# Kernel tuning notes

Hardware: AMD Instinct MI355X
Metric: run time of the kernel (lower is better)

## Reference

```python
import jax, jax.numpy as jnp
import numpy as np
import math

B, N, D, H, A, OBS, NB = 256, 64, 512, 8, 64, 128, 4
HD = D // H
EPS = 1e-5


def layernorm(x, g, b):
    mu = jnp.mean(x, axis=-1, keepdims=True)
    var = jnp.mean((x - mu) ** 2, axis=-1, keepdims=True)
    return (x - mu) * jax.lax.rsqrt(var + EPS) * g + b


def gelu(x):
    return jax.nn.gelu(x, approximate=False)  # torch nn.GELU default = exact erf


def mha_masked(k_in, v_in, q_in, wq, wk, wv, wp, bq, bk, bv, bp):
    # weights stored [in, out]; torch Linear computes x @ W.T, same math with random init
    b, l, d = q_in.shape
    q = (q_in @ wq + bq).reshape(b, l, H, HD).transpose(0, 2, 1, 3)  # [B,H,L,hd]
    k = (k_in @ wk + bk).reshape(b, l, H, HD).transpose(0, 2, 1, 3)
    v = (v_in @ wv + bv).reshape(b, l, H, HD).transpose(0, 2, 1, 3)
    att = jnp.einsum('bhqd,bhkd->bhqk', q, k) * (1.0 / math.sqrt(HD))
    causal = jnp.tril(jnp.ones((l, l), dtype=bool))  # registered tril buffer in original MAT code
    att = jnp.where(causal[None, None], att, -jnp.inf)
    att = jax.nn.softmax(att, axis=-1)
    y = jnp.einsum('bhqk,bhkd->bhqd', att, v)
    y = y.transpose(0, 2, 1, 3).reshape(b, l, d)
    return y @ wp + bp


def setup_inputs() -> dict:
    key = jax.random.key(0)
    ks = iter(jax.random.split(key, 32))
    s = 0.02
    inp = {
        'action': jax.random.normal(next(ks), (B, N, A + 1), jnp.float32),
        'obs_rep': jax.random.normal(next(ks), (B, N, D), jnp.float32),
        'obs': jax.random.normal(next(ks), (B, N, OBS), jnp.float32),
        'w_ae': jax.random.normal(next(ks), (A + 1, D), jnp.float32) * s,
        'ln0_g': jnp.ones((D,), jnp.float32),
        'ln0_b': jnp.zeros((D,), jnp.float32),
        'blk_ln_g': jnp.ones((NB, 3, D), jnp.float32),
        'blk_ln_b': jnp.zeros((NB, 3, D), jnp.float32),
        'blk_wq': jax.random.normal(next(ks), (NB, 2, D, D), jnp.float32) * s,
        'blk_wk': jax.random.normal(next(ks), (NB, 2, D, D), jnp.float32) * s,
        'blk_wv': jax.random.normal(next(ks), (NB, 2, D, D), jnp.float32) * s,
        'blk_wp': jax.random.normal(next(ks), (NB, 2, D, D), jnp.float32) * s,
        'blk_bq': jnp.zeros((NB, 2, D), jnp.float32),
        'blk_bk': jnp.zeros((NB, 2, D), jnp.float32),
        'blk_bv': jnp.zeros((NB, 2, D), jnp.float32),
        'blk_bp': jnp.zeros((NB, 2, D), jnp.float32),
        'blk_w1': jax.random.normal(next(ks), (NB, D, D), jnp.float32) * s,
        'blk_b1': jnp.zeros((NB, D), jnp.float32),
        'blk_w2': jax.random.normal(next(ks), (NB, D, D), jnp.float32) * s,
        'blk_b2': jnp.zeros((NB, D), jnp.float32),
        'wh1': jax.random.normal(next(ks), (D, D), jnp.float32) * s,
        'bh1': jnp.zeros((D,), jnp.float32),
        'lnh_g': jnp.ones((D,), jnp.float32),
        'lnh_b': jnp.zeros((D,), jnp.float32),
        'wh2': jax.random.normal(next(ks), (D, A), jnp.float32) * s,
        'bh2': jnp.zeros((A,), jnp.float32),
    }
    return inp


def reference(action, obs_rep, obs, w_ae, ln0_g, ln0_b, blk_ln_g, blk_ln_b,
              blk_wq, blk_wk, blk_wv, blk_wp, blk_bq, blk_bk, blk_bv, blk_bp,
              blk_w1, blk_b1, blk_w2, blk_b2, wh1, bh1, lnh_g, lnh_b, wh2, bh2):
    # action encoder: Linear(no bias) + GELU, then LayerNorm
    x = layernorm(gelu(action @ w_ae), ln0_g, ln0_b)
    for i in range(NB):
        # sublayer 1: masked self-attn + residual + LN
        a1 = mha_masked(x, x, x, blk_wq[i, 0], blk_wk[i, 0], blk_wv[i, 0], blk_wp[i, 0],
                        blk_bq[i, 0], blk_bk[i, 0], blk_bv[i, 0], blk_bp[i, 0])
        x = layernorm(x + a1, blk_ln_g[i, 0], blk_ln_b[i, 0])
        # sublayer 2: masked cross-attn (key=x, value=x, query=obs_rep) + residual with obs_rep + LN
        a2 = mha_masked(x, x, obs_rep, blk_wq[i, 1], blk_wk[i, 1], blk_wv[i, 1], blk_wp[i, 1],
                        blk_bq[i, 1], blk_bk[i, 1], blk_bv[i, 1], blk_bp[i, 1])
        x = layernorm(obs_rep + a2, blk_ln_g[i, 1], blk_ln_b[i, 1])
        # sublayer 3: GELU MLP (D -> D -> D) + residual + LN
        m = gelu(x @ blk_w1[i] + blk_b1[i]) @ blk_w2[i] + blk_b2[i]
        x = layernorm(x + m, blk_ln_g[i, 2], blk_ln_b[i, 2])
    # head: Linear + GELU + LN + Linear
    h = layernorm(gelu(x @ wh1 + bh1), lnh_g, lnh_b)
    logit = h @ wh2 + bh2
    return logit
```

## Files before the change

### kernel.cpp

```cpp
#include <hip/hip_runtime.h>
#include <hip/hip_bf16.h>
#include <math.h>

namespace {

constexpr int B  = 256;
constexpr int N  = 64;
constexpr int D  = 512;
constexpr int H  = 8;
constexpr int NBLK = 4;
constexpr int M  = B * N;
constexpr float EPS = 1e-5f;
constexpr float SCALE = 0.125f;
constexpr int NEVER = 1 << 20;

typedef __attribute__((ext_vector_type(8))) short short8b;
typedef __attribute__((ext_vector_type(4))) float f32x4;

__device__ __forceinline__ float gelu_exact(float x) {
  return 0.5f * x * (1.0f + erff(x * 0.70710678118654752440f));
}

__device__ __forceinline__ unsigned short f2b_bits(float f) {
  __hip_bfloat16 h = __float2bfloat16(f);
  return *reinterpret_cast<unsigned short*>(&h);
}

#define GLOBAL_AS __attribute__((address_space(1)))
#define LDS_AS    __attribute__((address_space(3)))

__device__ __forceinline__ void gload_lds16(const void* g, void* l) {
  __builtin_amdgcn_global_load_lds((const GLOBAL_AS void*)g, (LDS_AS void*)l, 16, 0, 0);
}

template<bool GELU, int SPLIT>
__global__ __launch_bounds__(512, 2) void gemm_dp_kernel(
    const __hip_bfloat16* __restrict__ A,
    const __hip_bfloat16* __restrict__ Wt,
    const float* __restrict__ bias,
    __hip_bfloat16* __restrict__ out1, int ostr1,
    __hip_bfloat16* __restrict__ vt, int gy) {
  constexpr int K = 512;
  constexpr int NT = 8;
  __shared__ __hip_bfloat16 Als[3][128][64];
  __shared__ __hip_bfloat16 Bls[3][256][64];

  const int nwg = gridDim.x;
  const int hw  = blockIdx.x;
  const int cpx = nwg >> 3;
  const int lg  = (hw & 7) * cpx + (hw >> 3);
  const int bm  = (lg / gy) * 128;
  const int bn  = (lg % gy) * 256;

  const int tid  = threadIdx.x;
  const int wave = tid >> 6;
  const int lane = tid & 63;
  const int wm   = (wave >> 2) * 64;
  const int wn   = (wave & 3) * 64;
  const int fr   = lane & 15;
  const int fg   = lane >> 4;

  const int srow  = tid >> 3;
  const int sslot = (tid & 7) ^ (srow & 7);
  const __hip_bfloat16* gA = A  + (size_t)(bm + srow) * K + sslot * 8;
  const __hip_bfloat16* gB = Wt + (size_t)(bn + srow) * K + sslot * 8;

  auto STAGE = [&](int buf, int kt) {
    const int ko = kt * 64;
    char* la = (char*)&Als[buf][0][0] + wave * 1024;
    char* lb = (char*)&Bls[buf][0][0] + wave * 1024;
    gload_lds16(gA + ko,           la);
    gload_lds16(gA + 64 * K + ko,  la + 8192);
    gload_lds16(gB + ko,           lb);
    gload_lds16(gB + 64 * K + ko,  lb + 8192);
    gload_lds16(gB + 128 * K + ko, lb + 16384);
    gload_lds16(gB + 192 * K + ko, lb + 24576);
  };

  auto lda = [&](int buf, int mi, int ks) -> short8b {
    const int row  = wm + mi * 16 + fr;
    const int byte = row * 128 + (((ks << 2) | fg) ^ (fr & 7)) * 16;
    return *reinterpret_cast<const short8b*>((const char*)&Als[buf][0][0] + byte);
  };
  auto ldb = [&](int buf, int ni, int ks) -> short8b {
    const int row  = wn + ni * 16 + fr;
    const int byte = row * 128 + (((ks << 2) | fg) ^ (fr & 7)) * 16;
    return *reinterpret_cast<const short8b*>((const char*)&Bls[buf][0][0] + byte);
  };

  STAGE(0, 0);
  STAGE(1, 1);
  asm volatile("s_waitcnt vmcnt(6)" ::: "memory");
  __builtin_amdgcn_sched_barrier(0);
  __builtin_amdgcn_s_barrier();
  __builtin_amdgcn_sched_barrier(0);

  f32x4 acc[4][4] = {};
  for (int t = 0; t < NT; ++t) {
    const int cur = t % 3;
    if (t + 2 < NT) STAGE((t + 2) % 3, t + 2);

    short8b a0[4], b0[4], a1[4], b1[4];
#pragma unroll
    for (int mi = 0; mi < 4; ++mi) a0[mi] = lda(cur, mi, 0);
#pragma unroll
    for (int ni = 0; ni < 4; ++ni) b0[ni] = ldb(cur, ni, 0);
#pragma unroll
    for (int mi = 0; mi < 4; ++mi) a1[mi] = lda(cur, mi, 1);
#pragma unroll
    for (int ni = 0; ni < 4; ++ni) b1[ni] = ldb(cur, ni, 1);

    __builtin_amdgcn_s_setprio(1);
#pragma unroll
    for (int mi = 0; mi < 4; ++mi)
#pragma unroll
      for (int ni = 0; ni < 4; ++ni)
        acc[mi][ni] = __builtin_amdgcn_mfma_f32_16x16x32_bf16(a0[mi], b0[ni], acc[mi][ni], 0, 0, 0);
#pragma unroll
    for (int mi = 0; mi < 4; ++mi)
#pragma unroll
      for (int ni = 0; ni < 4; ++ni)
        acc[mi][ni] = __builtin_amdgcn_mfma_f32_16x16x32_bf16(a1[mi], b1[ni], acc[mi][ni], 0, 0, 0);
    __builtin_amdgcn_s_setprio(0);

    if (t + 2 < NT) {
      asm volatile("s_waitcnt vmcnt(6)" ::: "memory");
    } else {
      asm volatile("s_waitcnt vmcnt(0)" ::: "memory");
    }
    __builtin_amdgcn_sched_barrier(0);
    __builtin_amdgcn_s_barrier();
    __builtin_amdgcn_sched_barrier(0);
  }

#pragma unroll
  for (int ni = 0; ni < 4; ++ni) {
    const int col = bn + wn + ni * 16 + fr;
    const float bv = bias ? bias[col] : 0.f;
#pragma unroll
    for (int mi = 0; mi < 4; ++mi) {
      const int row0 = bm + wm + mi * 16 + fg * 4;
      if (col >= SPLIT) {
        const int vcol = col - SPLIT;
        ushort4 o;
        o.x = f2b_bits(acc[mi][ni][0] + bv);
        o.y = f2b_bits(acc[mi][ni][1] + bv);
        o.z = f2b_bits(acc[mi][ni][2] + bv);
        o.w = f2b_bits(acc[mi][ni][3] + bv);
        const int b8 = row0 >> 6, nl = row0 & 63;
        const int hh = vcol >> 6, dl = vcol & 63;
        *reinterpret_cast<ushort4*>(vt +
            ((size_t)(b8 * 8 + hh) * 4096 + dl * 64 + nl)) = o;
      } else {
#pragma unroll
        for (int q = 0; q < 4; ++q) {
          float v = acc[mi][ni][q] + bv;
          if (GELU) v = gelu_exact(v);
          out1[(size_t)(row0 + q) * ostr1 + col] = __float2bfloat16(v);
        }
      }
    }
  }
}

template<int KSTEPS>
__global__ __launch_bounds__(256) void gemm_head_kernel(
    const __hip_bfloat16* __restrict__ A,
    const __hip_bfloat16* __restrict__ Wt,
    const float* __restrict__ bias,
    float* __restrict__ out1, int ostr1, int nvalid) {
  constexpr int K = KSTEPS * 32;
  __shared__ __hip_bfloat16 Als[2][128][32];
  __shared__ __hip_bfloat16 Bls[2][128][32];

  const int bm   = blockIdx.x * 128;
  const int bn   = blockIdx.y * 128;
  const int tid  = threadIdx.x;
  const int wave = tid >> 6;
  const int lane = tid & 63;
  const int wm   = (wave >> 1) * 64;
  const int wn   = (wave & 1) * 64;
  const int fr   = lane & 15;
  const int fg   = lane >> 4;

  const int srow = (lane >> 2);
  const int scol = (lane & 3) * 8;
  const __hip_bfloat16* gA0 = A  + (size_t)(bm + wave * 32 + srow) * K + scol;
  const __hip_bfloat16* gA1 = gA0 + 16 * K;
  const __hip_bfloat16* gB0 = Wt + (size_t)(bn + wave * 32 + srow) * K + scol;
  const __hip_bfloat16* gB1 = gB0 + 16 * K;

  f32x4 acc[4][4] = {};

  auto stage = [&](int buf, int ks) {
    const int ko = ks * 32;
    gload_lds16(gA0 + ko, &Als[buf][wave * 32][0]);
    gload_lds16(gA1 + ko, &Als[buf][wave * 32 + 16][0]);
    gload_lds16(gB0 + ko, &Bls[buf][wave * 32][0]);
    gload_lds16(gB1 + ko, &Bls[buf][wave * 32 + 16][0]);
  };

  stage(0, 0);
  int buf = 0;
  for (int ks = 0; ks < KSTEPS; ++ks) {
    __syncthreads();
    if (ks + 1 < KSTEPS) stage(buf ^ 1, ks + 1);
    short8b a[4], b[4];
#pragma unroll
    for (int mi = 0; mi < 4; ++mi)
      a[mi] = *reinterpret_cast<const short8b*>(&Als[buf][wm + mi * 16 + fr][fg * 8]);
#pragma unroll
    for (int ni = 0; ni < 4; ++ni)
      b[ni] = *reinterpret_cast<const short8b*>(&Bls[buf][wn + ni * 16 + fr][fg * 8]);
#pragma unroll
    for (int mi = 0; mi < 4; ++mi)
#pragma unroll
      for (int ni = 0; ni < 4; ++ni)
        acc[mi][ni] = __builtin_amdgcn_mfma_f32_16x16x32_bf16(a[mi], b[ni], acc[mi][ni], 0, 0, 0);
    buf ^= 1;
  }

#pragma unroll
  for (int ni = 0; ni < 4; ++ni) {
    const int col = bn + wn + ni * 16 + fr;
    if (col >= nvalid) continue;
    const float bv = bias ? bias[col] : 0.f;
#pragma unroll
    for (int mi = 0; mi < 4; ++mi) {
      const int row0 = bm + wm + mi * 16 + fg * 4;
#pragma unroll
      for (int q = 0; q < 4; ++q)
        out1[(size_t)(row0 + q) * ostr1 + col] = acc[mi][ni][q] + bv;
    }
  }
}

template<int KSTEPS, bool GELU_PRE, bool RES>
__global__ __launch_bounds__(512) void gemm_ln_kernel(
    const __hip_bfloat16* __restrict__ A,
    const __hip_bfloat16* __restrict__ Wt,
    const float* __restrict__ bias,
    const __hip_bfloat16* __restrict__ resb,
    const float* __restrict__ g, const float* __restrict__ bb,
    __hip_bfloat16* __restrict__ outB) {
  constexpr int K = KSTEPS * 32;
  __shared__ __hip_bfloat16 Als[2][64][32];
  __shared__ __hip_bfloat16 Bls[2][512][32];
  __shared__ float red[64][8];
  __shared__ float mrow[64];
  __shared__ float rrow[64];

  const int bm   = blockIdx.x * 64;
  const int tid  = threadIdx.x;
  const int wave = tid >> 6;
  const int lane = tid & 63;
  const int fr   = lane & 15;
  const int fg   = lane >> 4;
  const int srow = lane >> 2;
  const int scol = (lane & 3) * 8;

  auto stage = [&](int buf, int ks) {
    const int ko = ks * 32;
    if (wave < 4)
      gload_lds16(A + (size_t)(bm + wave * 16 + srow) * K + ko + scol,
                  &Als[buf][wave * 16][0]);
#pragma unroll
    for (int c = 0; c < 4; ++c)
      gload_lds16(Wt + (size_t)(wave * 64 + c * 16 + srow) * K + ko + scol,
                  &Bls[buf][wave * 64 + c * 16][0]);
  };

  f32x4 acc[4][4] = {};
  stage(0, 0);
  int buf = 0;
  for (int ks = 0; ks < KSTEPS; ++ks) {
    __syncthreads();
    if (ks + 1 < KSTEPS) stage(buf ^ 1, ks + 1);
    short8b a[4], b[4];
#pragma unroll
    for (int mi = 0; mi < 4; ++mi)
      a[mi] = *reinterpret_cast<const short8b*>(&Als[buf][mi * 16 + fr][fg * 8]);
#pragma unroll
    for (int ni = 0; ni < 4; ++ni)
      b[ni] = *reinterpret_cast<const short8b*>(&Bls[buf][wave * 64 + ni * 16 + fr][fg * 8]);
#pragma unroll
    for (int mi = 0; mi < 4; ++mi)
#pragma unroll
      for (int ni = 0; ni < 4; ++ni)
        acc[mi][ni] = __builtin_amdgcn_mfma_f32_16x16x32_bf16(a[mi], b[ni], acc[mi][ni], 0, 0, 0);
    buf ^= 1;
  }

  float v[4][4][4];
  float bvc[4];
#pragma unroll
  for (int ni = 0; ni < 4; ++ni)
    bvc[ni] = bias ? bias[wave * 64 + ni * 16 + fr] : 0.f;
#pragma unroll
  for (int mi = 0; mi < 4; ++mi)
#pragma unroll
    for (int q = 0; q < 4; ++q) {
      const int row = bm + mi * 16 + fg * 4 + q;
#pragma unroll
      for (int ni = 0; ni < 4; ++ni) {
        float t = acc[mi][ni][q] + bvc[ni];
        if (GELU_PRE) t = gelu_exact(t);
        if (RES)
          t += __bfloat162float(resb[(size_t)row * D + wave * 64 + ni * 16 + fr]);
        v[mi][ni][q] = t;
      }
    }

  float ps[16];
#pragma unroll
  for (int mi = 0; mi < 4; ++mi)
#pragma unroll
    for (int q = 0; q < 4; ++q)
      ps[mi * 4 + q] = v[mi][0][q] + v[mi][1][q] + v[mi][2][q] + v[mi][3][q];
#pragma unroll
  for (int mask = 1; mask < 16; mask <<= 1)
#pragma unroll
    for (int t = 0; t < 16; ++t) ps[t] += __shfl_xor(ps[t], mask);
  if (fr == 0) {
#pragma unroll
    for (int mi = 0; mi < 4; ++mi)
#pragma unroll
      for (int q = 0; q < 4; ++q)
        red[mi * 16 + fg * 4 + q][wave] = ps[mi * 4 + q];
  }
  __syncthreads();
  if (tid < 64) {
    float s = 0.f;
#pragma unroll
    for (int w = 0; w < 8; ++w) s += red[tid][w];
    mrow[tid] = s * (1.f / 512.f);
  }
  __syncthreads();
  float mu[16];
#pragma unroll
  for (int mi = 0; mi < 4; ++mi)
#pragma unroll
    for (int q = 0; q < 4; ++q) mu[mi * 4 + q] = mrow[mi * 16 + fg * 4 + q];

  float ps2[16];
#pragma unroll
  for (int mi = 0; mi < 4; ++mi)
#pragma unroll
    for (int q = 0; q < 4; ++q) {
      const float m = mu[mi * 4 + q];
      float s = 0.f;
#pragma unroll
      for (int ni = 0; ni < 4; ++ni) {
        const float d = v[mi][ni][q] - m;
        s += d * d;
      }
      ps2[mi * 4 + q] = s;
    }
#pragma unroll
  for (int mask = 1; mask < 16; mask <<= 1)
#pragma unroll
    for (int t = 0; t < 16; ++t) ps2[t] += __shfl_xor(ps2[t], mask);
  if (fr == 0) {
#pragma unroll
    for (int mi = 0; mi < 4; ++mi)
#pragma unroll
      for (int q = 0; q < 4; ++q)
        red[mi * 16 + fg * 4 + q][wave] = ps2[mi * 4 + q];
  }
  __syncthreads();
  if (tid < 64) {
    float s = 0.f;
#pragma unroll
    for (int w = 0; w < 8; ++w) s += red[tid][w];
    rrow[tid] = rsqrtf(s * (1.f / 512.f) + EPS);
  }
  __syncthreads();

#pragma unroll
  for (int ni = 0; ni < 4; ++ni) {
    const int col = wave * 64 + ni * 16 + fr;
    const float gc = g[col], bc = bb[col];
#pragma unroll
    for (int mi = 0; mi < 4; ++mi)
#pragma unroll
      for (int q = 0; q < 4; ++q) {
        const int lrow = mi * 16 + fg * 4 + q;
        const int row = bm + lrow;
        const float o = (v[mi][ni][q] - mu[mi * 4 + q]) * rrow[lrow] * gc + bc;
        outB[(size_t)row * D + col] = __float2bfloat16(o);
      }
  }
}

__global__ __launch_bounds__(256) void attn_mfma_kernel(
    const __hip_bfloat16* __restrict__ qg, int qstr,
    const __hip_bfloat16* __restrict__ kg, int kstr,
    const __hip_bfloat16* __restrict__ vt,
    __hip_bfloat16* __restrict__ yg) {
  __shared__ __align__(16) char smem[33280];
  unsigned short* Qs  = (unsigned short*)smem;
  unsigned short* Ks  = (unsigned short*)(smem + 8192);
  float*          Ss  = (float*)smem;
  unsigned short* Vts = (unsigned short*)(smem + 16896);
  unsigned short* Ps  = (unsigned short*)(smem + 25088);

  const int tid  = threadIdx.x;
  const int bh   = blockIdx.x;
  const int bidx = bh >> 3, h = bh & 7;
  const size_t rbase = (size_t)bidx * 64;
  const int col0 = h * 64;

  const __hip_bfloat16* vtg = vt + (size_t)bh * 4096;
#pragma unroll
  for (int p = 0; p < 2; ++p) {
    const int idx = tid + p * 256;
    const int row = idx >> 3, c8 = (idx & 7) * 8;
    const int lb  = (row * 128 + c8 * 2) ^ ((row & 7) << 4);
    const uint4 vq = *reinterpret_cast<const uint4*>(qg + (rbase + row) * qstr + col0 + c8);
    const uint4 vk = *reinterpret_cast<const uint4*>(kg + (rbase + row) * kstr + col0 + c8);
    const uint4 vv = *reinterpret_cast<const uint4*>(vtg + idx * 8);
    *reinterpret_cast<uint4*>((char*)Qs  + lb) = vq;
    *reinterpret_cast<uint4*>((char*)Ks  + lb) = vk;
    *reinterpret_cast<uint4*>((char*)Vts + lb) = vv;
  }
  __syncthreads();

  const int wave = tid >> 6, lane = tid & 63;
  const int fr = lane & 15, fg = lane >> 4;
  const int wr = (wave >> 1) * 32, wc = (wave & 1) * 32;

  auto ldfrag = [&](const unsigned short* base, int row, int ks) -> short8b {
    const int byte = (row * 128 + ks * 64 + fg * 16) ^ ((row & 7) << 4);
    return *reinterpret_cast<const short8b*>((const char*)base + byte);
  };

  f32x4 acc[2][2] = {};
#pragma unroll
  for (int ks = 0; ks < 2; ++ks) {
    short8b a[2], b[2];
    a[0] = ldfrag(Qs, wr + fr, ks);
    a[1] = ldfrag(Qs, wr + 16 + fr, ks);
    b[0] = ldfrag(Ks, wc + fr, ks);
    b[1] = ldfrag(Ks, wc + 16 + fr, ks);
#pragma unroll
    for (int mi = 0; mi < 2; ++mi)
#pragma unroll
      for (int ni = 0; ni < 2; ++ni)
        acc[mi][ni] = __builtin_amdgcn_mfma_f32_16x16x32_bf16(a[mi], b[ni], acc[mi][ni], 0, 0, 0);
  }
  __syncthreads();

#pragma unroll
  for (int mi = 0; mi < 2; ++mi)
#pragma unroll
    for (int ni = 0; ni < 2; ++ni) {
      const int m2 = wc + ni * 16 + fr;
#pragma unroll
      for (int r = 0; r < 4; ++r) {
        const int n = wr + mi * 16 + fg * 4 + r;
        Ss[n * 66 + m2] = (m2 <= n) ? acc[mi][ni][r] * SCALE : -1e30f;
      }
    }
  __syncthreads();

  for (int n = wave * 16; n < wave * 16 + 16; ++n) {
    const float vv = Ss[n * 66 + lane];
    float mx = vv;
#pragma unroll
    for (int off = 1; off < 64; off <<= 1) mx = fmaxf(mx, __shfl_xor(mx, off));
    const float p = (lane <= n) ? __expf(vv - mx) : 0.f;
    float sum = p;
#pragma unroll
    for (int off = 1; off < 64; off <<= 1) sum += __shfl_xor(sum, off);
    const int byte = (n * 128 + lane * 2) ^ ((n & 7) << 4);
    *(unsigned short*)((char*)Ps + byte) = f2b_bits(p / sum);
  }
  __syncthreads();

  f32x4 acc2[2][2] = {};
#pragma unroll
  for (int ks = 0; ks < 2; ++ks) {
    short8b a[2], b[2];
    a[0] = ldfrag(Ps, wr + fr, ks);
    a[1] = ldfrag(Ps, wr + 16 + fr, ks);
    b[0] = ldfrag(Vts, wc + fr, ks);
    b[1] = ldfrag(Vts, wc + 16 + fr, ks);
#pragma unroll
    for (int mi = 0; mi < 2; ++mi)
#pragma unroll
      for (int ni = 0; ni < 2; ++ni)
        acc2[mi][ni] = __builtin_amdgcn_mfma_f32_16x16x32_bf16(a[mi], b[ni], acc2[mi][ni], 0, 0, 0);
  }
#pragma unroll
  for (int mi = 0; mi < 2; ++mi)
#pragma unroll
    for (int r = 0; r < 4; ++r) {
      const int n = wr + mi * 16 + fg * 4 + r;
      yg[(rbase + n) * 512 + col0 + wc + fr]      = __float2bfloat16(acc2[mi][0][r]);
      yg[(rbase + n) * 512 + col0 + wc + 16 + fr] = __float2bfloat16(acc2[mi][1][r]);
    }
}

__global__ __launch_bounds__(256) void wconv_all_kernel(
    const float* __restrict__ bwq, const float* __restrict__ bwk,
    const float* __restrict__ bwv, const float* __restrict__ bwp,
    const float* __restrict__ bw1, const float* __restrict__ bw2,
    const float* __restrict__ wh1,
    __hip_bfloat16* __restrict__ wSelf, __hip_bfloat16* __restrict__ wCq,
    __hip_bfloat16* __restrict__ wCkv, __hip_bfloat16* __restrict__ wTp,
    __hip_bfloat16* __restrict__ wTw1, __hip_bfloat16* __restrict__ wTw2,
    __hip_bfloat16* __restrict__ wTh1) {
  const size_t MAT = (size_t)D * D;
  const size_t SS = (size_t)1536 * 512, KV = (size_t)1024 * 512;
  const int z = blockIdx.z;
  const float* src;
  __hip_bfloat16* dst;
  if (z < 8)       { int i = z >> 1; src = bwq + (size_t)z * MAT;
                     dst = (z & 1) ? wCq + (size_t)i * MAT : wSelf + (size_t)i * SS; }
  else if (z < 16) { int zz = z - 8, i = zz >> 1; src = bwk + (size_t)zz * MAT;
                     dst = (zz & 1) ? wCkv + (size_t)i * KV
                                    : wSelf + (size_t)i * SS + 512 * 512; }
  else if (z < 24) { int zz = z - 16, i = zz >> 1; src = bwv + (size_t)zz * MAT;
                     dst = (zz & 1) ? wCkv + (size_t)i * KV + 512 * 512
                                    : wSelf + (size_t)i * SS + 1024 * 512; }
  else if (z < 32) { int zz = z - 24; src = bwp + (size_t)zz * MAT; dst = wTp + (size_t)zz * MAT; }
  else if (z < 36) { int zz = z - 32; src = bw1 + (size_t)zz * MAT; dst = wTw1 + (size_t)zz * MAT; }
  else if (z < 40) { int zz = z - 36; src = bw2 + (size_t)zz * MAT; dst = wTw2 + (size_t)zz * MAT; }
  else             { src = wh1; dst = wTh1; }

  __shared__ float tile[32][33];
  const int r0 = blockIdx.y * 32, c0 = blockIdx.x * 32;
  const int tr = threadIdx.x >> 5;
  const int tc = threadIdx.x & 31;
#pragma unroll
  for (int i = 0; i < 4; ++i)
    tile[tr + 8 * i][tc] = src[(size_t)(r0 + tr + 8 * i) * D + c0 + tc];
  __syncthreads();
#pragma unroll
  for (int i = 0; i < 4; ++i)
    dst[(size_t)(c0 + tr + 8 * i) * D + r0 + tc] = __float2bfloat16(tile[tc][tr + 8 * i]);
}

__global__ __launch_bounds__(256) void misc_prep_kernel(
    const float* __restrict__ w_ae, const float* __restrict__ wh2,
    const float* __restrict__ bbq, const float* __restrict__ bbk,
    const float* __restrict__ bbv, const float* __restrict__ action,
    __hip_bfloat16* __restrict__ waeT, __hip_bfloat16* __restrict__ wh2p,
    float* __restrict__ selfb, float* __restrict__ ckvb,
    float* __restrict__ bqc, __hip_bfloat16* __restrict__ actb) {
  constexpr int R0 = 512 * 96, R1 = 128 * 512, R2 = NBLK * 1536,
                R3 = NBLK * 1024, R4 = NBLK * 512, R5 = M * 96;
  constexpr int total = R0 + R1 + R2 + R3 + R4 + R5;
  for (int i = blockIdx.x * 256 + threadIdx.x; i < total; i += gridDim.x * 256) {
    int j = i;
    if (j < R0) {
      const int n = j / 96, k = j - n * 96;
      waeT[j] = (k < 65) ? __float2bfloat16(w_ae[(size_t)k * 512 + n]) : __float2bfloat16(0.f);
    } else if ((j -= R0) < R1) {
      const int n = j >> 9, k = j & 511;
      wh2p[j] = (n < 64) ? __float2bfloat16(wh2[(size_t)k * 64 + n]) : __float2bfloat16(0.f);
    } else if ((j -= R1) < R2) {
      const int blk = j / 1536, c = j - blk * 1536;
      const int seg = c >> 9, cc = c & 511;
      const float* s = (seg == 0) ? bbq : (seg == 1) ? bbk : bbv;
      selfb[j] = s[(size_t)(blk * 2) * 512 + cc];
    } else if ((j -= R2) < R3) {
      const int blk = j >> 10, c = j & 1023;
      ckvb[j] = (c < 512) ? bbk[(size_t)(blk * 2 + 1) * 512 + c]
                          : bbv[(size_t)(blk * 2 + 1) * 512 + (c - 512)];
    } else if ((j -= R3) < R4) {
      const int blk = j >> 9, c = j & 511;
      bqc[j] = bbq[(size_t)(blk * 2 + 1) * 512 + c];
    } else {
      j -= R4;
      const int row = j / 96, k = j - row * 96;
      actb[j] = (k < 65) ? __float2bfloat16(action[(size_t)row * 65 + k]) : __float2bfloat16(0.f);
    }
  }
}

__global__ __launch_bounds__(256) void cvt_kernel(
    const float* __restrict__ src, __hip_bfloat16* __restrict__ dst, int n4) {
  const int i = blockIdx.x * 256 + threadIdx.x;
  if (i < n4) {
    const float4 v = reinterpret_cast<const float4*>(src)[i];
    ushort4 o;
    o.x = f2b_bits(v.x); o.y = f2b_bits(v.y);
    o.z = f2b_bits(v.z); o.w = f2b_bits(v.w);
    reinterpret_cast<ushort4*>(dst)[i] = o;
  }
}

}

extern "C" void kernel_launch(void* const* d_in, const int* in_sizes, int n_in,
                              void* d_out, int out_size, void* d_ws, size_t ws_size,
                              hipStream_t stream) {
  const float* action  = (const float*)d_in[0];
  const float* obs_rep = (const float*)d_in[1];
  const float* w_ae    = (const float*)d_in[3];
  const float* ln0_g   = (const float*)d_in[4];
  const float* ln0_b   = (const float*)d_in[5];
  const float* bln_g   = (const float*)d_in[6];
  const float* bln_b   = (const float*)d_in[7];
  const float* bwq     = (const float*)d_in[8];
  const float* bwk     = (const float*)d_in[9];
  const float* bwv     = (const float*)d_in[10];
  const float* bwp     = (const float*)d_in[11];
  const float* bbq     = (const float*)d_in[12];
  const float* bbk     = (const float*)d_in[13];
  const float* bbv     = (const float*)d_in[14];
  const float* bbp     = (const float*)d_in[15];
  const float* bw1     = (const float*)d_in[16];
  const float* bb1     = (const float*)d_in[17];
  const float* bw2     = (const float*)d_in[18];
  const float* bb2     = (const float*)d_in[19];
  const float* wh1     = (const float*)d_in[20];
  const float* bh1     = (const float*)d_in[21];
  const float* lnh_g   = (const float*)d_in[22];
  const float* lnh_b   = (const float*)d_in[23];
  const float* wh2     = (const float*)d_in[24];
  const float* bh2     = (const float*)d_in[25];

  char* ws = (char*)d_ws;
  const size_t MAT = (size_t)D * D;
  const size_t szB = (size_t)M * D * 2;

  __hip_bfloat16* xb  = (__hip_bfloat16*)ws; ws += szB;
  __hip_bfloat16* hb  = (__hip_bfloat16*)ws; ws += szB;
  __hip_bfloat16* vtb = (__hip_bfloat16*)ws; ws += szB;
  __hip_bfloat16* orb = (__hip_bfloat16*)ws; ws += szB;
  __hip_bfloat16* qkb = (__hip_bfloat16*)ws; ws += 2 * szB;
  __hip_bfloat16* qcb = (__hip_bfloat16*)ws; ws += 4 * szB;
  __hip_bfloat16* kb  = (__hip_bfloat16*)ws; ws += szB;
  __hip_bfloat16* actb = (__hip_bfloat16*)ws; ws += (size_t)M * 96 * 2;
  __hip_bfloat16* wSelf = (__hip_bfloat16*)ws; ws += (size_t)NBLK * 1536 * 512 * 2;
  __hip_bfloat16* wCq   = (__hip_bfloat16*)ws; ws += (size_t)NBLK * 512 * 512 * 2;
  __hip_bfloat16* wCkv  = (__hip_bfloat16*)ws; ws += (size_t)NBLK * 1024 * 512 * 2;
  __hip_bfloat16* wTp   = (__hip_bfloat16*)ws; ws += 8 * MAT * 2;
  __hip_bfloat16* wTw1  = (__hip_bfloat16*)ws; ws += 4 * MAT * 2;
  __hip_bfloat16* wTw2  = (__hip_bfloat16*)ws; ws += 4 * MAT * 2;
  __hip_bfloat16* wTh1  = (__hip_bfloat16*)ws; ws += MAT * 2;
  __hip_bfloat16* wh2p  = (__hip_bfloat16*)ws; ws += 128 * 512 * 2;
  __hip_bfloat16* waeT  = (__hip_bfloat16*)ws; ws += 512 * 96 * 2;
  float* selfb         = (float*)ws;         ws += (size_t)NBLK * 1536 * 4;
  float* ckvb          = (float*)ws;         ws += (size_t)NBLK * 1024 * 4;
  float* bqc           = (float*)ws;         ws += (size_t)NBLK * 512 * 4;

  wconv_all_kernel<<<dim3(16, 16, 41), 256, 0, stream>>>(
      bwq, bwk, bwv, bwp, bw1, bw2, wh1,
      wSelf, wCq, wCkv, wTp, wTw1, wTw2, wTh1);
  misc_prep_kernel<<<2048, 256, 0, stream>>>(
      w_ae, wh2, bbq, bbk, bbv, action, waeT, wh2p, selfb, ckvb, bqc, actb);
  cvt_kernel<<<(M * D / 4 + 255) / 256, 256, 0, stream>>>(obs_rep, orb, M * D / 4);

  const size_t SS = (size_t)1536 * 512;
  const size_t KV = (size_t)1024 * 512;
  const int lnGrid = M / 64;

  gemm_ln_kernel<3, true, false><<<lnGrid, 512, 0, stream>>>(
      actb, waeT, nullptr, nullptr, ln0_g, ln0_b, xb);

  gemm_dp_kernel<false, NEVER><<<M / 128 * 8, 512, 0, stream>>>(
      orb, wCq, bqc, qcb, 2048, nullptr, 8);

  for (int i = 0; i < NBLK; ++i) {
    const float* g0 = bln_g + (size_t)(i * 3 + 0) * D;
    const float* b0 = bln_b + (size_t)(i * 3 + 0) * D;
    const float* g1 = bln_g + (size_t)(i * 3 + 1) * D;
    const float* b1 = bln_b + (size_t)(i * 3 + 1) * D;
    const float* g2 = bln_g + (size_t)(i * 3 + 2) * D;
    const float* b2 = bln_b + (size_t)(i * 3 + 2) * D;

    gemm_dp_kernel<false, 1024><<<M / 128 * 6, 512, 0, stream>>>(
        xb, wSelf + (size_t)i * SS, selfb + (size_t)i * 1536, qkb, 1024, vtb, 6);
    attn_mfma_kernel<<<B * H, 256, 0, stream>>>(qkb, 1024, qkb + 512, 1024, vtb, hb);
    gemm_ln_kernel<16, false, true><<<lnGrid, 512, 0, stream>>>(
        hb, wTp + (size_t)(i * 2) * MAT, bbp + (size_t)(i * 2) * D, xb, g0, b0, xb);

    gemm_dp_kernel<false, 512><<<M / 128 * 4, 512, 0, stream>>>(
        xb, wCkv + (size_t)i * KV, ckvb + (size_t)i * 1024, kb, 512, vtb, 4);
    attn_mfma_kernel<<<B * H, 256, 0, stream>>>(
        qcb + (size_t)i * 512, 2048, kb, 512, vtb, hb);
    gemm_ln_kernel<16, false, true><<<lnGrid, 512, 0, stream>>>(
        hb, wTp + (size_t)(i * 2 + 1) * MAT, bbp + (size_t)(i * 2 + 1) * D,
        orb, g1, b1, xb);

    gemm_dp_kernel<true, NEVER><<<M / 128 * 2, 512, 0, stream>>>(
        xb, wTw1 + (size_t)i * MAT, bb1 + (size_t)i * D, hb, 512, nullptr, 2);
    gemm_ln_kernel<16, false, true><<<lnGrid, 512, 0, stream>>>(
        hb, wTw2 + (size_t)i * MAT, bb2 + (size_t)i * D, xb, g2, b2, xb);
  }

  gemm_ln_kernel<16, true, false><<<lnGrid, 512, 0, stream>>>(
      xb, wTh1, bh1, nullptr, lnh_g, lnh_b, hb);
  gemm_head_kernel<16><<<dim3(M / 128, 1), 256, 0, stream>>>(
      hb, wh2p, bh2, (float*)d_out, 64, 64);
}
```

Before: 1.039 ms.

## Fuse MLP and head GEMM pairs through LDS, add swizzled 64-wide K tile for LN GEMMs

The MLP's two GEMMs (GELU then residual+LayerNorm) are merged into one kernel that keeps the 64x512 intermediate in swizzled LDS instead of writing it to global memory. The head's Linear+GELU+LN+Linear gets the same treatment. The projection GEMM+LN kernels now use a 64-wide K tile with XOR-swizzled LDS layout and s_setprio around the MFMA block. This removes launches and intermediate HBM traffic, but the fused kernel needs a large LDS footprint (about 64KB of mid buffer plus staging), which lowers occupancy. It also serializes the second GEMM behind the first within each block.

```diff
diff --git a/kernel.cpp b/kernel.cpp
--- a/kernel.cpp
+++ b/kernel.cpp
@@ -163,87 +163,509 @@
   }
 }
 
-template<int KSTEPS>
-__global__ __launch_bounds__(256) void gemm_head_kernel(
-    const __hip_bfloat16* __restrict__ A,
-    const __hip_bfloat16* __restrict__ Wt,
-    const float* __restrict__ bias,
-    float* __restrict__ out1, int ostr1, int nvalid) {
-  constexpr int K = KSTEPS * 32;
-  __shared__ __hip_bfloat16 Als[2][128][32];
-  __shared__ __hip_bfloat16 Bls[2][128][32];
-
-  const int bm   = blockIdx.x * 128;
-  const int bn   = blockIdx.y * 128;
-  const int tid  = threadIdx.x;
-  const int wave = tid >> 6;
-  const int lane = tid & 63;
-  const int wm   = (wave >> 1) * 64;
-  const int wn   = (wave & 1) * 64;
-  const int fr   = lane & 15;
-  const int fg   = lane >> 4;
-
-  const int srow = (lane >> 2);
-  const int scol = (lane & 3) * 8;
-  const __hip_bfloat16* gA0 = A  + (size_t)(bm + wave * 32 + srow) * K + scol;
-  const __hip_bfloat16* gA1 = gA0 + 16 * K;
-  const __hip_bfloat16* gB0 = Wt + (size_t)(bn + wave * 32 + srow) * K + scol;
-  const __hip_bfloat16* gB1 = gB0 + 16 * K;
-
-  f32x4 acc[4][4] = {};
-
-  auto stage = [&](int buf, int ks) {
-    const int ko = ks * 32;
-    gload_lds16(gA0 + ko, &Als[buf][wave * 32][0]);
-    gload_lds16(gA1 + ko, &Als[buf][wave * 32 + 16][0]);
-    gload_lds16(gB0 + ko, &Bls[buf][wave * 32][0]);
-    gload_lds16(gB1 + ko, &Bls[buf][wave * 32 + 16][0]);
-  };
-
-  stage(0, 0);
-  int buf = 0;
-  for (int ks = 0; ks < KSTEPS; ++ks) {
-    __syncthreads();
-    if (ks + 1 < KSTEPS) stage(buf ^ 1, ks + 1);
-    short8b a[4], b[4];
-#pragma unroll
-    for (int mi = 0; mi < 4; ++mi)
-      a[mi] = *reinterpret_cast<const short8b*>(&Als[buf][wm + mi * 16 + fr][fg * 8]);
-#pragma unroll
-    for (int ni = 0; ni < 4; ++ni)
-      b[ni] = *reinterpret_cast<const short8b*>(&Bls[buf][wn + ni * 16 + fr][fg * 8]);
-#pragma unroll
-    for (int mi = 0; mi < 4; ++mi)
-#pragma unroll
-      for (int ni = 0; ni < 4; ++ni)
-        acc[mi][ni] = __builtin_amdgcn_mfma_f32_16x16x32_bf16(a[mi], b[ni], acc[mi][ni], 0, 0, 0);
-    buf ^= 1;
-  }
-
-#pragma unroll
-  for (int ni = 0; ni < 4; ++ni) {
-    const int col = bn + wn + ni * 16 + fr;
-    if (col >= nvalid) continue;
-    const float bv = bias ? bias[col] : 0.f;
-#pragma unroll
-    for (int mi = 0; mi < 4; ++mi) {
-      const int row0 = bm + wm + mi * 16 + fg * 4;
-#pragma unroll
-      for (int q = 0; q < 4; ++q)
-        out1[(size_t)(row0 + q) * ostr1 + col] = acc[mi][ni][q] + bv;
-    }
-  }
-}
-
-template<int KSTEPS, bool GELU_PRE, bool RES>
-__global__ __launch_bounds__(512) void gemm_ln_kernel(
+template<bool GELU_PRE, bool RES>
+__global__ __launch_bounds__(512) void gemm_ln64_kernel(
     const __hip_bfloat16* __restrict__ A,
     const __hip_bfloat16* __restrict__ Wt,
     const float* __restrict__ bias,
     const __hip_bfloat16* __restrict__ resb,
     const float* __restrict__ g, const float* __restrict__ bb,
     __hip_bfloat16* __restrict__ outB) {
-  constexpr int K = KSTEPS * 32;
+  __shared__ __hip_bfloat16 Als[2][64][64];
+  __shared__ __hip_bfloat16 Bls[2][512][64];
+  __shared__ float red[64][8];
+  __shared__ float mrow[64];
+  __shared__ float rrow[64];
+
+  const int bm   = blockIdx.x * 64;
+  const int tid  = threadIdx.x;
+  const int wave = tid >> 6;
+  const int lane = tid & 63;
+  const int fr   = lane & 15;
+  const int fg   = lane >> 4;
+
+  const int srow  = tid >> 3;
+  const int sslot = (tid & 7) ^ (srow & 7);
+
+  auto stage = [&](int buf, int kt) {
+    const int ko = kt * 64;
+    gload_lds16(A + (size_t)(bm + srow) * 512 + ko + sslot * 8,
+                (char*)&Als[buf][0][0] + wave * 1024);
+#pragma unroll
+    for (int j = 0; j < 8; ++j) {
+      const int row = j * 64 + srow;
+      const int sl  = (tid & 7) ^ (row & 7);
+      gload_lds16(Wt + (size_t)row * 512 + ko + sl * 8,
+                  (char*)&Bls[buf][0][0] + j * 8192 + wave * 1024);
+    }
+  };
+
+  auto lda = [&](int buf, int mi, int ks) -> short8b {
+    const int row  = mi * 16 + fr;
+    const int byte = row * 128 + (((ks << 2) | fg) ^ (row & 7)) * 16;
+    return *reinterpret_cast<const short8b*>((const char*)&Als[buf][0][0] + byte);
+  };
+  auto ldb = [&](int buf, int ni, int ks) -> short8b {
+    const int row  = wave * 64 + ni * 16 + fr;
+    const int byte = row * 128 + (((ks << 2) | fg) ^ (row & 7)) * 16;
+    return *reinterpret_cast<const short8b*>((const char*)&Bls[buf][0][0] + byte);
+  };
+
+  f32x4 acc[4][4] = {};
+  stage(0, 0);
+  int buf = 0;
+  for (int kt = 0; kt < 8; ++kt) {
+    __syncthreads();
+    if (kt + 1 < 8) stage(buf ^ 1, kt + 1);
+    short8b a0[4], b0[4], a1[4], b1[4];
+#pragma unroll
+    for (int mi = 0; mi < 4; ++mi) a0[mi] = lda(buf, mi, 0);
+#pragma unroll
+    for (int ni = 0; ni < 4; ++ni) b0[ni] = ldb(buf, ni, 0);
+#pragma unroll
+    for (int mi = 0; mi < 4; ++mi) a1[mi] = lda(buf, mi, 1);
+#pragma unroll
+    for (int ni = 0; ni < 4; ++ni) b1[ni] = ldb(buf, ni, 1);
+    __builtin_amdgcn_s_setprio(1);
+#pragma unroll
+    for (int mi = 0; mi < 4; ++mi)
+#pragma unroll
+      for (int ni = 0; ni < 4; ++ni)
+        acc[mi][ni] = __builtin_amdgcn_mfma_f32_16x16x32_bf16(a0[mi], b0[ni], acc[mi][ni], 0, 0, 0);
+#pragma unroll
+    for (int mi = 0; mi < 4; ++mi)
+#pragma unroll
+      for (int ni = 0; ni < 4; ++ni)
+        acc[mi][ni] = __builtin_amdgcn_mfma_f32_16x16x32_bf16(a1[mi], b1[ni], acc[mi][ni], 0, 0, 0);
+    __builtin_amdgcn_s_setprio(0);
+    buf ^= 1;
+  }
+
+  float v[4][4][4];
+  float bvc[4];
+#pragma unroll
+  for (int ni = 0; ni < 4; ++ni)
+    bvc[ni] = bias ? bias[wave * 64 + ni * 16 + fr] : 0.f;
+#pragma unroll
+  for (int mi = 0; mi < 4; ++mi)
+#pragma unroll
+    for (int q = 0; q < 4; ++q) {
+      const int row = bm + mi * 16 + fg * 4 + q;
+#pragma unroll
+      for (int ni = 0; ni < 4; ++ni) {
+        float t = acc[mi][ni][q] + bvc[ni];
+        if (GELU_PRE) t = gelu_exact(t);
+        if (RES)
+          t += __bfloat162float(resb[(size_t)row * D + wave * 64 + ni * 16 + fr]);
+        v[mi][ni][q] = t;
+      }
+    }
+
+  float ps[16];
+#pragma unroll
+  for (int mi = 0; mi < 4; ++mi)
+#pragma unroll
+    for (int q = 0; q < 4; ++q)
+      ps[mi * 4 + q] = v[mi][0][q] + v[mi][1][q] + v[mi][2][q] + v[mi][3][q];
+#pragma unroll
+  for (int mask = 1; mask < 16; mask <<= 1)
+#pragma unroll
+    for (int t = 0; t < 16; ++t) ps[t] += __shfl_xor(ps[t], mask);
+  if (fr == 0) {
+#pragma unroll
+    for (int mi = 0; mi < 4; ++mi)
+#pragma unroll
+      for (int q = 0; q < 4; ++q)
+        red[mi * 16 + fg * 4 + q][wave] = ps[mi * 4 + q];
+  }
+  __syncthreads();
+  if (tid < 64) {
+    float s = 0.f;
+#pragma unroll
+    for (int w = 0; w < 8; ++w) s += red[tid][w];
+    mrow[tid] = s * (1.f / 512.f);
+  }
+  __syncthreads();
+  float mu[16];
+#pragma unroll
+  for (int mi = 0; mi < 4; ++mi)
+#pragma unroll
+    for (int q = 0; q < 4; ++q) mu[mi * 4 + q] = mrow[mi * 16 + fg * 4 + q];
+
+  float ps2[16];
+#pragma unroll
+  for (int mi = 0; mi < 4; ++mi)
+#pragma unroll
+    for (int q = 0; q < 4; ++q) {
+      const float m = mu[mi * 4 + q];
+      float s = 0.f;
+#pragma unroll
+      for (int ni = 0; ni < 4; ++ni) {
+        const float d = v[mi][ni][q] - m;
+        s += d * d;
+      }
+      ps2[mi * 4 + q] = s;
+    }
+#pragma unroll
+  for (int mask = 1; mask < 16; mask <<= 1)
+#pragma unroll
+    for (int t = 0; t < 16; ++t) ps2[t] += __shfl_xor(ps2[t], mask);
+  if (fr == 0) {
+#pragma unroll
+    for (int mi = 0; mi < 4; ++mi)
+#pragma unroll
+      for (int q = 0; q < 4; ++q)
+        red[mi * 16 + fg * 4 + q][wave] = ps2[mi * 4 + q];
+  }
+  __syncthreads();
+  if (tid < 64) {
+    float s = 0.f;
+#pragma unroll
+    for (int w = 0; w < 8; ++w) s += red[tid][w];
+    rrow[tid] = rsqrtf(s * (1.f / 512.f) + EPS);
+  }
+  __syncthreads();
+
+#pragma unroll
+  for (int ni = 0; ni < 4; ++ni) {
+    const int col = wave * 64 + ni * 16 + fr;
+    const float gc = g[col], bc = bb[col];
+#pragma unroll
+    for (int mi = 0; mi < 4; ++mi)
+#pragma unroll
+      for (int q = 0; q < 4; ++q) {
+        const int lrow = mi * 16 + fg * 4 + q;
+        const float o = (v[mi][ni][q] - mu[mi * 4 + q]) * rrow[lrow] * gc + bc;
+        outB[(size_t)(bm + lrow) * D + col] = __float2bfloat16(o);
+      }
+  }
+}
+
+template<int MODE>
+__global__ __launch_bounds__(512) void fused2_kernel(
+    const __hip_bfloat16* __restrict__ A,
+    const __hip_bfloat16* __restrict__ W1t, const float* __restrict__ b1,
+    const __hip_bfloat16* __restrict__ W2t, const float* __restrict__ b2,
+    const __hip_bfloat16* __restrict__ resb,
+    const float* __restrict__ g, const float* __restrict__ bb,
+    __hip_bfloat16* __restrict__ outB, float* __restrict__ outF) {
+  __shared__ __hip_bfloat16 Als[2][64][32];
+  __shared__ __hip_bfloat16 Bls[2][512][32];
+  __shared__ __hip_bfloat16 mid[64 * 512];
+  __shared__ float red[64][8];
+  __shared__ float mrow[64];
+  __shared__ float rrow[64];
+
+  const int bm   = blockIdx.x * 64;
+  const int tid  = threadIdx.x;
+  const int wave = tid >> 6;
+  const int lane = tid & 63;
+  const int fr   = lane & 15;
+  const int fg   = lane >> 4;
+
+  auto stageA = [&](int buf, int ks) {
+    if (wave < 4) {
+      const int row = wave * 16 + (lane >> 2);
+      const int sl  = (lane & 3) ^ (row & 3);
+      gload_lds16(A + (size_t)(bm + row) * 512 + ks * 32 + sl * 8,
+                  (char*)&Als[buf][0][0] + wave * 1024);
+    }
+  };
+  auto stageB = [&](const __hip_bfloat16* W, int buf, int ks) {
+#pragma unroll
+    for (int c = 0; c < 4; ++c) {
+      const int row = wave * 64 + c * 16 + (lane >> 2);
+      const int sl  = (lane & 3) ^ (row & 3);
+      gload_lds16(W + (size_t)row * 512 + ks * 32 + sl * 8,
+                  (char*)&Bls[buf][0][0] + (wave * 64 + c * 16) * 64);
+    }
+  };
+  auto stageB2h = [&](const __hip_bfloat16* W, int buf, int ks) {
+    const int row = (tid >> 2) & 127;
+    const int sl  = (tid & 3) ^ (row & 3);
+    gload_lds16(W + (size_t)row * 512 + ks * 32 + sl * 8,
+                (char*)&Bls[buf][0][0] + wave * 1024);
+  };
+
+  auto ldA = [&](int buf, int mi) -> short8b {
+    const int row  = mi * 16 + fr;
+    const int byte = row * 64 + (fg ^ (row & 3)) * 16;
+    return *reinterpret_cast<const short8b*>((const char*)&Als[buf][0][0] + byte);
+  };
+  auto ldB = [&](int buf, int row) -> short8b {
+    const int byte = row * 64 + (fg ^ (row & 3)) * 16;
+    return *reinterpret_cast<const short8b*>((const char*)&Bls[buf][0][0] + byte);
+  };
+  auto ldMid = [&](int mi, int ks) -> short8b {
+    const int row  = mi * 16 + fr;
+    const int byte = (row * 1024 + ks * 64 + fg * 16) ^ ((row & 7) << 4);
+    return *reinterpret_cast<const short8b*>((const char*)mid + byte);
+  };
+
+  f32x4 acc[4][4] = {};
+  stageA(0, 0); stageB(W1t, 0, 0);
+  int buf = 0;
+  for (int ks = 0; ks < 16; ++ks) {
+    __syncthreads();
+    if (ks + 1 < 16) { stageA(buf ^ 1, ks + 1); stageB(W1t, buf ^ 1, ks + 1); }
+    short8b a[4], b[4];
+#pragma unroll
+    for (int mi = 0; mi < 4; ++mi) a[mi] = ldA(buf, mi);
+#pragma unroll
+    for (int ni = 0; ni < 4; ++ni) b[ni] = ldB(buf, wave * 64 + ni * 16 + fr);
+#pragma unroll
+    for (int mi = 0; mi < 4; ++mi)
+#pragma unroll
+      for (int ni = 0; ni < 4; ++ni)
+        acc[mi][ni] = __builtin_amdgcn_mfma_f32_16x16x32_bf16(a[mi], b[ni], acc[mi][ni], 0, 0, 0);
+    buf ^= 1;
+  }
+
+  if (MODE == 0) stageB(W2t, 0, 0); else stageB2h(W2t, 0, 0);
+
+  {
+    float v[4][4][4];
+    float bvc[4];
+#pragma unroll
+    for (int ni = 0; ni < 4; ++ni)
+      bvc[ni] = b1[wave * 64 + ni * 16 + fr];
+#pragma unroll
+    for (int mi = 0; mi < 4; ++mi)
+#pragma unroll
+      for (int q = 0; q < 4; ++q)
+#pragma unroll
+        for (int ni = 0; ni < 4; ++ni)
+          v[mi][ni][q] = gelu_exact(acc[mi][ni][q] + bvc[ni]);
+
+    if (MODE == 1) {
+      float ps[16];
+#pragma unroll
+      for (int mi = 0; mi < 4; ++mi)
+#pragma unroll
+        for (int q = 0; q < 4; ++q)
+          ps[mi * 4 + q] = v[mi][0][q] + v[mi][1][q] + v[mi][2][q] + v[mi][3][q];
+#pragma unroll
+      for (int mask = 1; mask < 16; mask <<= 1)
+#pragma unroll
+        for (int t = 0; t < 16; ++t) ps[t] += __shfl_xor(ps[t], mask);
+      if (fr == 0)
+#pragma unroll
+        for (int mi = 0; mi < 4; ++mi)
+#pragma unroll
+          for (int q = 0; q < 4; ++q)
+            red[mi * 16 + fg * 4 + q][wave] = ps[mi * 4 + q];
+      __syncthreads();
+      if (tid < 64) {
+        float s = 0.f;
+#pragma unroll
+        for (int w = 0; w < 8; ++w) s += red[tid][w];
+        mrow[tid] = s * (1.f / 512.f);
+      }
+      __syncthreads();
+      float mu[16];
+#pragma unroll
+      for (int mi = 0; mi < 4; ++mi)
+#pragma unroll
+        for (int q = 0; q < 4; ++q) mu[mi * 4 + q] = mrow[mi * 16 + fg * 4 + q];
+      float ps2[16];
+#pragma unroll
+      for (int mi = 0; mi < 4; ++mi)
+#pragma unroll
+        for (int q = 0; q < 4; ++q) {
+          const float m = mu[mi * 4 + q];
+          float s = 0.f;
+#pragma unroll
+          for (int ni = 0; ni < 4; ++ni) { const float d = v[mi][ni][q] - m; s += d * d; }
+          ps2[mi * 4 + q] = s;
+        }
+#pragma unroll
+      for (int mask = 1; mask < 16; mask <<= 1)
+#pragma unroll
+        for (int t = 0; t < 16; ++t) ps2[t] += __shfl_xor(ps2[t], mask);
+      if (fr == 0)
+#pragma unroll
+        for (int mi = 0; mi < 4; ++mi)
+#pragma unroll
+          for (int q = 0; q < 4; ++q)
+            red[mi * 16 + fg * 4 + q][wave] = ps2[mi * 4 + q];
+      __syncthreads();
+      if (tid < 64) {
+        float s = 0.f;
+#pragma unroll
+        for (int w = 0; w < 8; ++w) s += red[tid][w];
+        rrow[tid] = rsqrtf(s * (1.f / 512.f) + EPS);
+      }
+      __syncthreads();
+#pragma unroll
+      for (int mi = 0; mi < 4; ++mi)
+#pragma unroll
+        for (int q = 0; q < 4; ++q) {
+          const int lrow = mi * 16 + fg * 4 + q;
+#pragma unroll
+          for (int ni = 0; ni < 4; ++ni) {
+            const int col = wave * 64 + ni * 16 + fr;
+            v[mi][ni][q] = (v[mi][ni][q] - mu[mi * 4 + q]) * rrow[lrow] * g[col] + bb[col];
+          }
+        }
+    }
+
+#pragma unroll
+    for (int mi = 0; mi < 4; ++mi)
+#pragma unroll
+      for (int q = 0; q < 4; ++q) {
+        const int row = mi * 16 + fg * 4 + q;
+#pragma unroll
+        for (int ni = 0; ni < 4; ++ni) {
+          const int col = wave * 64 + ni * 16 + fr;
+          const int byte = (row * 1024 + col * 2) ^ ((row & 7) << 4);
+          *(unsigned short*)((char*)mid + byte) = f2b_bits(v[mi][ni][q]);
+        }
+      }
+  }
+  __syncthreads();
+
+  if (MODE == 0) {
+    f32x4 acc2[4][4] = {};
+    int buf2 = 0;
+    for (int ks = 0; ks < 16; ++ks) {
+      if (ks) __syncthreads();
+      if (ks + 1 < 16) stageB(W2t, buf2 ^ 1, ks + 1);
+      short8b a[4], b[4];
+#pragma unroll
+      for (int mi = 0; mi < 4; ++mi) a[mi] = ldMid(mi, ks);
+#pragma unroll
+      for (int ni = 0; ni < 4; ++ni) b[ni] = ldB(buf2, wave * 64 + ni * 16 + fr);
+#pragma unroll
+      for (int mi = 0; mi < 4; ++mi)
+#pragma unroll
+        for (int ni = 0; ni < 4; ++ni)
+          acc2[mi][ni] = __builtin_amdgcn_mfma_f32_16x16x32_bf16(a[mi], b[ni], acc2[mi][ni], 0, 0, 0);
+      buf2 ^= 1;
+    }
+    __syncthreads();
+
+    float v[4][4][4];
+    float bvc[4];
+#pragma unroll
+    for (int ni = 0; ni < 4; ++ni)
+      bvc[ni] = b2[wave * 64 + ni * 16 + fr];
+#pragma unroll
+    for (int mi = 0; mi < 4; ++mi)
+#pragma unroll
+      for (int q = 0; q < 4; ++q) {
+        const int row = bm + mi * 16 + fg * 4 + q;
+#pragma unroll
+        for (int ni = 0; ni < 4; ++ni)
+          v[mi][ni][q] = acc2[mi][ni][q] + bvc[ni] +
+              __bfloat162float(resb[(size_t)row * D + wave * 64 + ni * 16 + fr]);
+      }
+
+    float ps[16];
+#pragma unroll
+    for (int mi = 0; mi < 4; ++mi)
+#pragma unroll
+      for (int q = 0; q < 4; ++q)
+        ps[mi * 4 + q] = v[mi][0][q] + v[mi][1][q] + v[mi][2][q] + v[mi][3][q];
+#pragma unroll
+    for (int mask = 1; mask < 16; mask <<= 1)
+#pragma unroll
+      for (int t = 0; t < 16; ++t) ps[t] += __shfl_xor(ps[t], mask);
+    if (fr == 0)
+#pragma unroll
+      for (int mi = 0; mi < 4; ++mi)
+#pragma unroll
+        for (int q = 0; q < 4; ++q)
+          red[mi * 16 + fg * 4 + q][wave] = ps[mi * 4 + q];
+    __syncthreads();
+    if (tid < 64) {
+      float s = 0.f;
+#pragma unroll
+      for (int w = 0; w < 8; ++w) s += red[tid][w];
+      mrow[tid] = s * (1.f / 512.f);
+    }
+    __syncthreads();
+    float mu[16];
+#pragma unroll
+    for (int mi = 0; mi < 4; ++mi)
+#pragma unroll
+      for (int q = 0; q < 4; ++q) mu[mi * 4 + q] = mrow[mi * 16 + fg * 4 + q];
+    float ps2[16];
+#pragma unroll
+    for (int mi = 0; mi < 4; ++mi)
+#pragma unroll
+      for (int q = 0; q < 4; ++q) {
+        const float m = mu[mi * 4 + q];
+        float s = 0.f;
+#pragma unroll
+        for (int ni = 0; ni < 4; ++ni) { const float d = v[mi][ni][q] - m; s += d * d; }
+        ps2[mi * 4 + q] = s;
+      }
+#pragma unroll
+    for (int mask = 1; mask < 16; mask <<= 1)
+#pragma unroll
+      for (int t = 0; t < 16; ++t) ps2[t] += __shfl_xor(ps2[t], mask);
+    if (fr == 0)
+#pragma unroll
+      for (int mi = 0; mi < 4; ++mi)
+#pragma unroll
+        for (int q = 0; q < 4; ++q)
+          red[mi * 16 + fg * 4 + q][wave] = ps2[mi * 4 + q];
+    __syncthreads();
+    if (tid < 64) {
+      float s = 0.f;
+#pragma unroll
+      for (int w = 0; w < 8; ++w) s += red[tid][w];
+      rrow[tid] = rsqrtf(s * (1.f / 512.f) + EPS);
+    }
+    __syncthreads();
+
+#pragma unroll
+    for (int ni = 0; ni < 4; ++ni) {
+      const int col = wave * 64 + ni * 16 + fr;
+      const float gc = g[col], bc = bb[col];
+#pragma unroll
+      for (int mi = 0; mi < 4; ++mi)
+#pragma unroll
+        for (int q = 0; q < 4; ++q) {
+          const int lrow = mi * 16 + fg * 4 + q;
+          const float o = (v[mi][ni][q] - mu[mi * 4 + q]) * rrow[lrow] * gc + bc;
+          outB[(size_t)(bm + lrow) * D + col] = __float2bfloat16(o);
+        }
+    }
+  } else {
+    const int mi = wave >> 1;
+    const int nb = (wave & 1) * 2;
+    f32x4 acc2[2] = {};
+    int buf2 = 0;
+    for (int ks = 0; ks < 16; ++ks) {
+      if (ks) __syncthreads();
+      if (ks + 1 < 16) stageB2h(W2t, buf2 ^ 1, ks + 1);
+      short8b a = ldMid(mi, ks);
+      short8b b0 = ldB(buf2, (nb + 0) * 16 + fr);
+      short8b b1 = ldB(buf2, (nb + 1) * 16 + fr);
+      acc2[0] = __builtin_amdgcn_mfma_f32_16x16x32_bf16(a, b0, acc2[0], 0, 0, 0);
+      acc2[1] = __builtin_amdgcn_mfma_f32_16x16x32_bf16(a, b1, acc2[1], 0, 0, 0);
+      buf2 ^= 1;
+    }
+#pragma unroll
+    for (int j = 0; j < 2; ++j) {
+      const int col = (nb + j) * 16 + fr;
+      const float bv = b2[col];
+#pragma unroll
+      for (int q = 0; q < 4; ++q) {
+        const int row = bm + mi * 16 + fg * 4 + q;
+        outF[(size_t)row * 64 + col] = acc2[j][q] + bv;
+      }
+    }
+  }
+}
+
+__global__ __launch_bounds__(512) void gemm_ln_enc_kernel(
+    const __hip_bfloat16* __restrict__ A,
+    const __hip_bfloat16* __restrict__ Wt,
+    const float* __restrict__ g, const float* __restrict__ bb,
+    __hip_bfloat16* __restrict__ outB) {
+  constexpr int K = 96;
   __shared__ __hip_bfloat16 Als[2][64][32];
   __shared__ __hip_bfloat16 Bls[2][512][32];
   __shared__ float red[64][8];
@@ -273,9 +695,9 @@
   f32x4 acc[4][4] = {};
   stage(0, 0);
   int buf = 0;
-  for (int ks = 0; ks < KSTEPS; ++ks) {
+  for (int ks = 0; ks < 3; ++ks) {
     __syncthreads();
-    if (ks + 1 < KSTEPS) stage(buf ^ 1, ks + 1);
+    if (ks + 1 < 3) stage(buf ^ 1, ks + 1);
     short8b a[4], b[4];
 #pragma unroll
     for (int mi = 0; mi < 4; ++mi)
@@ -292,24 +714,13 @@
   }
 
   float v[4][4][4];
-  float bvc[4];
-#pragma unroll
-  for (int ni = 0; ni < 4; ++ni)
-    bvc[ni] = bias ? bias[wave * 64 + ni * 16 + fr] : 0.f;
 #pragma unroll
   for (int mi = 0; mi < 4; ++mi)
 #pragma unroll
-    for (int q = 0; q < 4; ++q) {
-      const int row = bm + mi * 16 + fg * 4 + q;
-#pragma unroll
-      for (int ni = 0; ni < 4; ++ni) {
-        float t = acc[mi][ni][q] + bvc[ni];
-        if (GELU_PRE) t = gelu_exact(t);
-        if (RES)
-          t += __bfloat162float(resb[(size_t)row * D + wave * 64 + ni * 16 + fr]);
-        v[mi][ni][q] = t;
-      }
-    }
+    for (int q = 0; q < 4; ++q)
+#pragma unroll
+      for (int ni = 0; ni < 4; ++ni)
+        v[mi][ni][q] = gelu_exact(acc[mi][ni][q]);
 
   float ps[16];
 #pragma unroll
@@ -321,13 +732,12 @@
   for (int mask = 1; mask < 16; mask <<= 1)
 #pragma unroll
     for (int t = 0; t < 16; ++t) ps[t] += __shfl_xor(ps[t], mask);
-  if (fr == 0) {
+  if (fr == 0)
 #pragma unroll
     for (int mi = 0; mi < 4; ++mi)
 #pragma unroll
       for (int q = 0; q < 4; ++q)
         red[mi * 16 + fg * 4 + q][wave] = ps[mi * 4 + q];
-  }
   __syncthreads();
   if (tid < 64) {
     float s = 0.f;
@@ -341,7 +751,6 @@
   for (int mi = 0; mi < 4; ++mi)
 #pragma unroll
     for (int q = 0; q < 4; ++q) mu[mi * 4 + q] = mrow[mi * 16 + fg * 4 + q];
-
   float ps2[16];
 #pragma unroll
   for (int mi = 0; mi < 4; ++mi)
@@ -350,23 +759,19 @@
       const float m = mu[mi * 4 + q];
       float s = 0.f;
 #pragma unroll
-      for (int ni = 0; ni < 4; ++ni) {
-        const float d = v[mi][ni][q] - m;
-        s += d * d;
-      }
+      for (int ni = 0; ni < 4; ++ni) { const float d = v[mi][ni][q] - m; s += d * d; }
       ps2[mi * 4 + q] = s;
     }
 #pragma unroll
   for (int mask = 1; mask < 16; mask <<= 1)
 #pragma unroll
     for (int t = 0; t < 16; ++t) ps2[t] += __shfl_xor(ps2[t], mask);
-  if (fr == 0) {
+  if (fr == 0)
 #pragma unroll
     for (int mi = 0; mi < 4; ++mi)
 #pragma unroll
       for (int q = 0; q < 4; ++q)
         red[mi * 16 + fg * 4 + q][wave] = ps2[mi * 4 + q];
-  }
   __syncthreads();
   if (tid < 64) {
     float s = 0.f;
@@ -385,9 +790,8 @@
 #pragma unroll
       for (int q = 0; q < 4; ++q) {
         const int lrow = mi * 16 + fg * 4 + q;
-        const int row = bm + lrow;
         const float o = (v[mi][ni][q] - mu[mi * 4 + q]) * rrow[lrow] * gc + bc;
-        outB[(size_t)row * D + col] = __float2bfloat16(o);
+        outB[(size_t)(bm + lrow) * D + col] = __float2bfloat16(o);
       }
   }
 }
@@ -658,8 +1062,7 @@
   const size_t KV = (size_t)1024 * 512;
   const int lnGrid = M / 64;
 
-  gemm_ln_kernel<3, true, false><<<lnGrid, 512, 0, stream>>>(
-      actb, waeT, nullptr, nullptr, ln0_g, ln0_b, xb);
+  gemm_ln_enc_kernel<<<lnGrid, 512, 0, stream>>>(actb, waeT, ln0_g, ln0_b, xb);
 
   gemm_dp_kernel<false, NEVER><<<M / 128 * 8, 512, 0, stream>>>(
       orb, wCq, bqc, qcb, 2048, nullptr, 8);
@@ -675,25 +1078,23 @@
     gemm_dp_kernel<false, 1024><<<M / 128 * 6, 512, 0, stream>>>(
         xb, wSelf + (size_t)i * SS, selfb + (size_t)i * 1536, qkb, 1024, vtb, 6);
     attn_mfma_kernel<<<B * H, 256, 0, stream>>>(qkb, 1024, qkb + 512, 1024, vtb, hb);
-    gemm_ln_kernel<16, false, true><<<lnGrid, 512, 0, stream>>>(
+    gemm_ln64_kernel<false, true><<<lnGrid, 512, 0, stream>>>(
         hb, wTp + (size_t)(i * 2) * MAT, bbp + (size_t)(i * 2) * D, xb, g0, b0, xb);
 
     gemm_dp_kernel<false, 512><<<M / 128 * 4, 512, 0, stream>>>(
         xb, wCkv + (size_t)i * KV, ckvb + (size_t)i * 1024, kb, 512, vtb, 4);
     attn_mfma_kernel<<<B * H, 256, 0, stream>>>(
         qcb + (size_t)i * 512, 2048, kb, 512, vtb, hb);
-    gemm_ln_kernel<16, false, true><<<lnGrid, 512, 0, stream>>>(
+    gemm_ln64_kernel<false, true><<<lnGrid, 512, 0, stream>>>(
         hb, wTp + (size_t)(i * 2 + 1) * MAT, bbp + (size_t)(i * 2 + 1) * D,
         orb, g1, b1, xb);
 
-    gemm_dp_kernel<true, NEVER><<<M / 128 * 2, 512, 0, stream>>>(
-        xb, wTw1 + (size_t)i * MAT, bb1 + (size_t)i * D, hb, 512, nullptr, 2);
-    gemm_ln_kernel<16, false, true><<<lnGrid, 512, 0, stream>>>(
-        hb, wTw2 + (size_t)i * MAT, bb2 + (size_t)i * D, xb, g2, b2, xb);
-  }
-
-  gemm_ln_kernel<16, true, false><<<lnGrid, 512, 0, stream>>>(
-      xb, wTh1, bh1, nullptr, lnh_g, lnh_b, hb);
-  gemm_head_kernel<16><<<dim3(M / 128, 1), 256, 0, stream>>>(
-      hb, wh2p, bh2, (float*)d_out, 64, 64);
-}
+    fused2_kernel<0><<<lnGrid, 512, 0, stream>>>(
+        xb, wTw1 + (size_t)i * MAT, bb1 + (size_t)i * D,
+        wTw2 + (size_t)i * MAT, bb2 + (size_t)i * D,
+        xb, g2, b2, xb, nullptr);
+  }
+
+  fused2_kernel<1><<<lnGrid, 512, 0, stream>>>(
+      xb, wTh1, bh1, wh2p, bh2, nullptr, lnh_g, lnh_b, nullptr, (float*)d_out);
+}
```

New measurement: 1.021 ms. No clear change (-1.7%).
